# Kernel optimization log

Measured on AMD Instinct MI355X. Metric: run time of the kernel, lower is better.

## Reference

```python
import jax, jax.numpy as jnp
import numpy as np

SCENE_MIN = -1.0
SCENE_SIZE = 2.0
BASE_RES = 64

# 8 child corner offsets (from subdivide_voxels), scaled by 0.25
_OFFSETS = jnp.array([[-1, -1, -1], [1, -1, -1], [-1, 1, -1], [1, 1, -1],
                      [-1, -1, 1], [1, -1, 1], [-1, 1, 1], [1, 1, 1]],
                     dtype=jnp.float32) * 0.25  # [8, 3]


def _part1by2(n):
    # vectorized bit-interleave: spread 10 bits of n so there are 2 zero bits between each
    n = n & jnp.uint32(0x3FF)
    n = (n ^ (n << 16)) & jnp.uint32(0xFF0000FF)
    n = (n ^ (n << 8)) & jnp.uint32(0x0300F00F)
    n = (n ^ (n << 4)) & jnp.uint32(0x030C30C3)
    n = (n ^ (n << 2)) & jnp.uint32(0x09249249)
    return n


def _morton3d(coords):
    # coords: [M, 3] uint32 -> [M] int32 Morton codes
    x, y, z = coords[:, 0], coords[:, 1], coords[:, 2]
    code = (_part1by2(z) << 2) + (_part1by2(y) << 1) + _part1by2(x)
    return code.astype(jnp.int32)


def setup_inputs() -> dict:
    key = jax.random.key(0)
    k1, k2, k3, k4 = jax.random.split(key, 4)
    N = 262144  # 64^3 base voxels
    positions = jax.random.uniform(k1, (N, 3), dtype=jnp.float32) * SCENE_SIZE + SCENE_MIN
    sizes = jax.random.uniform(k2, (N,), dtype=jnp.float32) * 0.03 + 0.001
    densities = jax.random.normal(k3, (N,), dtype=jnp.float32) * 0.1
    colors = jax.random.normal(k4, (N, 27), dtype=jnp.float32) * 0.1
    return {"positions": positions, "sizes": sizes, "densities": densities,
            "colors": colors, "level": 1}


def reference(positions, sizes, densities, colors, level):
    N = positions.shape[0]
    # subdivide all voxels: child_pos = parent_pos + offset * parent_size (offset already *0.25)
    child_pos = positions[:, None, :] + _OFFSETS[None, :, :] * sizes[:, None, None]  # [N,8,3]
    child_pos = child_pos.reshape(N * 8, 3)
    child_sizes = jnp.repeat(sizes * 0.5, 8)           # [8N]
    child_dens = jnp.repeat(densities, 8)              # [8N]
    child_colors = jnp.repeat(colors, 8, axis=0)       # [8N, 27]

    # Morton codes at child level
    grid_res = BASE_RES * (2 ** int(level))
    norm = (child_pos - SCENE_MIN) / SCENE_SIZE
    coords = jnp.clip((norm * grid_res).astype(jnp.int32), 0, grid_res - 1).astype(jnp.uint32)
    morton = _morton3d(coords)  # [8N] int32

    out = jnp.concatenate(
        [child_pos, child_sizes[:, None], child_dens[:, None], child_colors], axis=-1)  # [8N, 32]
    return out, morton
```

## Files before the change

kernel.cpp:

```cpp
#include <hip/hip_runtime.h>

typedef float f4 __attribute__((ext_vector_type(4)));

#define P   32
#define REC 36

__device__ __forceinline__ unsigned int part1by2(unsigned int n) {
    n &= 1023u;
    n = (n ^ (n << 16)) & 0xFF0000FFu;
    n = (n ^ (n << 8))  & 0x0300F00Fu;
    n = (n ^ (n << 4))  & 0x030C30C3u;
    n = (n ^ (n << 2))  & 0x09249249u;
    return n;
}

__global__ __launch_bounds__(256) void asv_kernel(
    const float* __restrict__ positions,
    const float* __restrict__ sizes,
    const float* __restrict__ densities,
    const float* __restrict__ colors,
    const int*   __restrict__ level_p,
    float* __restrict__ out,
    float* __restrict__ morton_out,
    int N)
{
    __shared__ float rec[P * REC];
    const int tid  = threadIdx.x;
    const int base = blockIdx.x * P;
    const int nloc = min(P, N - base);

    if (tid < nloc)
        rec[tid * REC + 3] = sizes[base + tid];
    if (tid >= 64 && tid < 64 + nloc)
        rec[(tid - 64) * REC + 4] = densities[base + (tid - 64)];
    if (tid >= 128 && tid < 128 + nloc * 3) {
        int k = tid - 128;
        rec[(k / 3) * REC + (k % 3)] = positions[(size_t)base * 3 + k];
    }
    for (int k = tid; k < nloc * 27; k += 256)
        rec[(k / 27) * REC + 5 + (k % 27)] = colors[(size_t)base * 27 + k];
    __syncthreads();

    const int kq = tid & 7;
    const int j  = (tid >> 3) & 7;
    const float sx = (j & 1) ? 0.25f : -0.25f;
    const float sy = (j & 2) ? 0.25f : -0.25f;
    const float sz = (j & 4) ? 0.25f : -0.25f;
    const int   gr  = 64 << level_p[0];
    const float grf = (float)gr;

    f4* __restrict__ outv = (f4*)out;
    const int qblock = blockIdx.x * (P * 64);

    #pragma unroll
    for (int u = 0; u < 8; ++u) {
        const int lq = u * 256 + tid;
        const int p  = lq >> 6;
        if (p < nloc) {
            f4 v = *(const f4*)&rec[p * REC + kq * 4];
            if (kq == 0) {
                const float px = v.x, py = v.y, pz = v.z, s = v.w;
                const float cx = __fadd_rn(px, sx * s);
                const float cy = __fadd_rn(py, sy * s);
                const float cz = __fadd_rn(pz, sz * s);

                int ix = (int)(__fmul_rn(__fmul_rn(__fadd_rn(cx, 1.0f), 0.5f), grf));
                int iy = (int)(__fmul_rn(__fmul_rn(__fadd_rn(cy, 1.0f), 0.5f), grf));
                int iz = (int)(__fmul_rn(__fmul_rn(__fadd_rn(cz, 1.0f), 0.5f), grf));
                ix = min(max(ix, 0), gr - 1);
                iy = min(max(iy, 0), gr - 1);
                iz = min(max(iz, 0), gr - 1);

                unsigned int code = (part1by2((unsigned)iz) << 2)
                                  | (part1by2((unsigned)iy) << 1)
                                  |  part1by2((unsigned)ix);
                morton_out[(qblock + lq) >> 3] = (float)(int)code;

                f4 w = {cx, cy, cz, 0.5f * s};
                v = w;
            }
            outv[qblock + lq] = v;
        }
    }
}

extern "C" void kernel_launch(void* const* d_in, const int* in_sizes, int n_in,
                              void* d_out, int out_size, void* d_ws, size_t ws_size,
                              hipStream_t stream) {
    const float* positions = (const float*)d_in[0];
    const float* sizes     = (const float*)d_in[1];
    const float* densities = (const float*)d_in[2];
    const float* colors    = (const float*)d_in[3];
    const int*   level_p   = (const int*)d_in[4];

    int N = in_sizes[1];
    float* out        = (float*)d_out;
    float* morton_out = out + (size_t)N * 8 * 32;

    int blocks = (N + P - 1) / P;
    asv_kernel<<<blocks, 256, 0, stream>>>(positions, sizes, densities, colors,
                                           level_p, out, morton_out, N);
}
```

Measured before the change: 67.40 us.

## Split Morton code computation into separate blocks and use nontemporal stores

Adds extra blocks to the grid, one thread per parent voxel. Each computes the Morton codes of all 8 children from shared per-axis cells and writes them as two 16-byte vector stores, replacing scattered 4-byte stores from the kq==0 lanes of the main loop. The main blocks now only compute child positions and sizes, and their output writes become nontemporal stores. The cost is a second read of positions and sizes, plus extra blocks that must finish after the main ones.

```diff
diff --git a/kernel.cpp b/kernel.cpp
--- a/kernel.cpp
+++ b/kernel.cpp
@@ -22,10 +22,44 @@
     const int*   __restrict__ level_p,
     float* __restrict__ out,
     float* __restrict__ morton_out,
-    int N)
+    int N, int mainBlocks)
 {
+    const int tid = threadIdx.x;
+    const int gr  = 64 << level_p[0];
+    const float grf = (float)gr;
+
+    if (blockIdx.x >= mainBlocks) {
+        const int i = (blockIdx.x - mainBlocks) * 256 + tid;
+        if (i >= N) return;
+        const float s  = sizes[i];
+        const float t  = 0.25f * s;
+        const float px = positions[3 * i + 0];
+        const float py = positions[3 * i + 1];
+        const float pz = positions[3 * i + 2];
+
+        #define CELL(c) ({                                                   \
+            int _v = (int)(__fmul_rn(__fmul_rn(__fadd_rn((c), 1.0f), 0.5f), grf)); \
+            _v = min(max(_v, 0), gr - 1);                                    \
+            part1by2((unsigned)_v); })
+        const unsigned bx0 = CELL(__fadd_rn(px, -t));
+        const unsigned bx1 = CELL(__fadd_rn(px,  t));
+        const unsigned by0 = CELL(__fadd_rn(py, -t)) << 1;
+        const unsigned by1 = CELL(__fadd_rn(py,  t)) << 1;
+        const unsigned bz0 = CELL(__fadd_rn(pz, -t)) << 2;
+        const unsigned bz1 = CELL(__fadd_rn(pz,  t)) << 2;
+        #undef CELL
+
+        f4 m0 = {(float)(int)(bz0 | by0 | bx0), (float)(int)(bz0 | by0 | bx1),
+                 (float)(int)(bz0 | by1 | bx0), (float)(int)(bz0 | by1 | bx1)};
+        f4 m1 = {(float)(int)(bz1 | by0 | bx0), (float)(int)(bz1 | by0 | bx1),
+                 (float)(int)(bz1 | by1 | bx0), (float)(int)(bz1 | by1 | bx1)};
+        f4* mp = (f4*)(morton_out + (size_t)i * 8);
+        __builtin_nontemporal_store(m0, mp);
+        __builtin_nontemporal_store(m1, mp + 1);
+        return;
+    }
+
     __shared__ float rec[P * REC];
-    const int tid  = threadIdx.x;
     const int base = blockIdx.x * P;
     const int nloc = min(P, N - base);
 
@@ -46,8 +80,6 @@
     const float sx = (j & 1) ? 0.25f : -0.25f;
     const float sy = (j & 2) ? 0.25f : -0.25f;
     const float sz = (j & 4) ? 0.25f : -0.25f;
-    const int   gr  = 64 << level_p[0];
-    const float grf = (float)gr;
 
     f4* __restrict__ outv = (f4*)out;
     const int qblock = blockIdx.x * (P * 64);
@@ -59,27 +91,13 @@
         if (p < nloc) {
             f4 v = *(const f4*)&rec[p * REC + kq * 4];
             if (kq == 0) {
-                const float px = v.x, py = v.y, pz = v.z, s = v.w;
-                const float cx = __fadd_rn(px, sx * s);
-                const float cy = __fadd_rn(py, sy * s);
-                const float cz = __fadd_rn(pz, sz * s);
-
-                int ix = (int)(__fmul_rn(__fmul_rn(__fadd_rn(cx, 1.0f), 0.5f), grf));
-                int iy = (int)(__fmul_rn(__fmul_rn(__fadd_rn(cy, 1.0f), 0.5f), grf));
-                int iz = (int)(__fmul_rn(__fmul_rn(__fadd_rn(cz, 1.0f), 0.5f), grf));
-                ix = min(max(ix, 0), gr - 1);
-                iy = min(max(iy, 0), gr - 1);
-                iz = min(max(iz, 0), gr - 1);
-
-                unsigned int code = (part1by2((unsigned)iz) << 2)
-                                  | (part1by2((unsigned)iy) << 1)
-                                  |  part1by2((unsigned)ix);
-                morton_out[(qblock + lq) >> 3] = (float)(int)code;
-
-                f4 w = {cx, cy, cz, 0.5f * s};
+                f4 w = {__fadd_rn(v.x, sx * v.w),
+                        __fadd_rn(v.y, sy * v.w),
+                        __fadd_rn(v.z, sz * v.w),
+                        0.5f * v.w};
                 v = w;
             }
-            outv[qblock + lq] = v;
+            __builtin_nontemporal_store(v, &outv[qblock + lq]);
         }
     }
 }
@@ -97,7 +115,9 @@
     float* out        = (float*)d_out;
     float* morton_out = out + (size_t)N * 8 * 32;
 
-    int blocks = (N + P - 1) / P;
-    asv_kernel<<<blocks, 256, 0, stream>>>(positions, sizes, densities, colors,
-                                           level_p, out, morton_out, N);
+    int mainBlocks   = (N + P - 1) / P;
+    int mortonBlocks = (N + 255) / 256;
+    asv_kernel<<<mainBlocks + mortonBlocks, 256, 0, stream>>>(
+        positions, sizes, densities, colors, level_p, out, morton_out,
+        N, mainBlocks);
 }
```

Result: faster. 57.34 us (-14.9%).
